# Optimization experiments

Measured on AMD Instinct MI355X. Metric: run time of the kernel, lower is better.

Reference implementation:

```python
import jax, jax.numpy as jnp
import numpy as np

B, P1, P2 = 16, 25, 24          # batch, patch-grid rows (+cls row), cols
E0, E1, E2 = 8, 8, 16           # 3-way factorized embed dim (total 1024)
H1, H2, H3 = 2, 2, 4            # 3-way head split (16 heads)
X, Y, Z = E0 // H1, E1 // H2, E2 // H3   # per-head factor dims (4,4,4)
SCALE = float((X * Y * Z) ** -0.5)        # head_dim = 64


def _tcl(x, w0, w1, w2, b):
    # Tensor Contraction Layer: mode-wise linear maps on the 3 embed modes.
    return jnp.einsum('bpqxyz,ax,cy,dz->bpqacd', x, w0, w1, w2) + b


def setup_inputs() -> dict:
    key = jax.random.key(0)
    ks = jax.random.split(key, 17)
    inp = {"x": jax.random.normal(ks[0], (B, P1, P2, E0, E1, E2), jnp.float32)}
    i = 1
    for nm in ("q", "k", "v", "o"):
        inp[f"{nm}_w0"] = jax.random.normal(ks[i], (E0, E0), jnp.float32) * (E0 ** -0.5); i += 1
        inp[f"{nm}_w1"] = jax.random.normal(ks[i], (E1, E1), jnp.float32) * (E1 ** -0.5); i += 1
        inp[f"{nm}_w2"] = jax.random.normal(ks[i], (E2, E2), jnp.float32) * (E2 ** -0.5); i += 1
        inp[f"{nm}_b"] = jax.random.normal(ks[i], (E0, E1, E2), jnp.float32) * 0.02; i += 1
    return inp


def _split_heads(t):
    t = t.reshape(B, P1, P2, X, H1, Y, H2, Z, H3)
    return t.transpose(0, 1, 2, 4, 6, 8, 3, 5, 7)


def reference(x,
              q_w0, q_w1, q_w2, q_b,
              k_w0, k_w1, k_w2, k_b,
              v_w0, v_w1, v_w2, v_b,
              o_w0, o_w1, o_w2, o_b):
    q = _tcl(x, q_w0, q_w1, q_w2, q_b)
    k = _tcl(x, k_w0, k_w1, k_w2, k_b)
    v = _tcl(x, v_w0, v_w1, v_w2, v_b)
    Q, K, V = _split_heads(q), _split_heads(k), _split_heads(v)
    # scores over all (p1,p2) x (m,n) token pairs, per (h1,h2,h3) head
    attn = jnp.einsum('bpqdefxyz,bmndefxyz->bdefpqmn', Q, K) * SCALE
    a = attn.reshape(B, H1, H2, H3, P1, P2, P1 * P2)
    a = jax.nn.softmax(a, axis=-1).reshape(attn.shape)
    out = jnp.einsum('bdefpqmn,bmndefxyz->bdefpqxyz', a, V)
    # b h1 h2 h3 p q x y z -> b p q (x h1)(y h2)(z h3)
    out = out.transpose(0, 4, 5, 6, 1, 7, 2, 8, 3).reshape(B, P1, P2, E0, E1, E2)
    return _tcl(out, o_w0, o_w1, o_w2, o_b)
```

## Files before the change

### kernel.cpp

```cpp
#include <hip/hip_runtime.h>

#define S   600
#define NB  16
#define NH  16
#define HD  64
#define QSCALE 0.18033688011112042f

#define LDT 20

typedef _Float16 f16x8 __attribute__((ext_vector_type(8)));
typedef float f32x4 __attribute__((ext_vector_type(4)));

__global__ __launch_bounds__(256) void tcl_qkv_kernel(
    const float* __restrict__ x,
    const float* __restrict__ qw0, const float* __restrict__ qw1,
    const float* __restrict__ qw2, const float* __restrict__ qb,
    const float* __restrict__ kw0, const float* __restrict__ kw1,
    const float* __restrict__ kw2, const float* __restrict__ kb,
    const float* __restrict__ vw0, const float* __restrict__ vw1,
    const float* __restrict__ vw2, const float* __restrict__ vb,
    _Float16* __restrict__ Qh, _Float16* __restrict__ Kh,
    _Float16* __restrict__ Vh)
{
  __shared__ __align__(16) float t1s[4][64 * LDT];
  __shared__ __align__(16) float t2s[4][64 * LDT];

  const int tid = threadIdx.x;
  const int wv = tid >> 6, lane = tid & 63;
  const int tok = blockIdx.x * 4 + wv;
  const int b = tok / S, t = tok - b * S;
  const int q = lane >> 3, zp = lane & 7;
  float* __restrict__ t1 = t1s[wv];
  float* __restrict__ t2 = t2s[wv];

  float2 xc[8];
  #pragma unroll
  for (int xx = 0; xx < 8; ++xx)
    xc[xx] = *(const float2*)&x[(size_t)tok * 1024 + xx * 128 + q * 16 + zp * 2];

  const int xs = lane >> 4;
  const int h1 = (lane >> 3) & 1;
  const int cc = lane & 7;
  const int ys = cc >> 1, h2 = cc & 1;

  const float* W0[3] = {qw0, kw0, vw0};
  const float* W1[3] = {qw1, kw1, vw1};
  const float* W2[3] = {qw2, kw2, vw2};
  const float* BB[3] = {qb, kb, vb};
  _Float16* OUT[3] = {Qh, Kh, Vh};

  #pragma unroll
  for (int p = 0; p < 3; ++p) {
    const float* __restrict__ w0 = W0[p];
    const float* __restrict__ w1 = W1[p];
    const float* __restrict__ w2 = W2[p];
    const float* __restrict__ bb = BB[p];
    _Float16* __restrict__ op = OUT[p];

    #pragma unroll
    for (int a = 0; a < 8; ++a) {
      float2 r = make_float2(0.f, 0.f);
      #pragma unroll
      for (int xx = 0; xx < 8; ++xx) {
        const float w = w0[a * 8 + xx];
        r.x = fmaf(w, xc[xx].x, r.x);
        r.y = fmaf(w, xc[xx].y, r.y);
      }
      *(float2*)&t1[(a * 8 + q) * LDT + zp * 2] = r;
    }
    __builtin_amdgcn_wave_barrier();

    float2 t1r[8];
    #pragma unroll
    for (int y = 0; y < 8; ++y)
      t1r[y] = *(float2*)&t1[(q * 8 + y) * LDT + zp * 2];
    #pragma unroll
    for (int c = 0; c < 8; ++c) {
      float2 r = make_float2(0.f, 0.f);
      #pragma unroll
      for (int y = 0; y < 8; ++y) {
        const float w = w1[c * 8 + y];
        r.x = fmaf(w, t1r[y].x, r.x);
        r.y = fmaf(w, t1r[y].y, r.y);
      }
      *(float2*)&t2[(q * 8 + c) * LDT + zp * 2] = r;
    }
    __builtin_amdgcn_wave_barrier();

    float t2r[16];
    #pragma unroll
    for (int k = 0; k < 4; ++k)
      *(float4*)&t2r[k * 4] = *(float4*)&t2[lane * LDT + k * 4];
    float bias[16];
    #pragma unroll
    for (int k = 0; k < 4; ++k)
      *(float4*)&bias[k * 4] = *(const float4*)&bb[lane * 16 + k * 4];
    float o[16];
    #pragma unroll
    for (int d = 0; d < 16; ++d) {
      float acc = 0.f;
      #pragma unroll
      for (int j = 0; j < 16; ++j)
        acc = fmaf(w2[d * 16 + j], t2r[j], acc);
      o[d] = acc + bias[d];
    }
    const float sc = (p == 0) ? QSCALE : 1.0f;
    #pragma unroll
    for (int h3 = 0; h3 < 4; ++h3) {
      union { _Float16 hh[4]; uint2 u; } pk;
      #pragma unroll
      for (int z = 0; z < 4; ++z)
        pk.hh[z] = (_Float16)(o[4 * z + h3] * sc);
      const int head = h1 * 8 + h2 * 4 + h3;
      *(uint2*)&op[((size_t)((b * NH + head) * S + t)) * HD + xs * 16 + ys * 4]
          = pk.u;
    }
    __builtin_amdgcn_wave_barrier();
  }
}

__global__ __launch_bounds__(256) void vtrans_kernel(
    const _Float16* __restrict__ Vh, _Float16* __restrict__ Vt)
{
  __shared__ __align__(16) _Float16 tile[64 * 64];
  const int tid = threadIdx.x;
  const int tt = blockIdx.x, h = blockIdx.y, b = blockIdx.z;
  const size_t rbase = (size_t)(b * NH + h) * S * HD;
  const size_t wbase = (size_t)(b * NH + h) * HD * S;
  const int t0 = tt * 64;

  #pragma unroll
  for (int hp = 0; hp < 2; ++hp) {
    const int u = hp * 256 + tid;
    const int r = u >> 3, ch = u & 7;
    f16x8 v = {0, 0, 0, 0, 0, 0, 0, 0};
    if (t0 + r < S) v = *(const f16x8*)&Vh[rbase + (size_t)(t0 + r) * HD + ch * 8];
    *(f16x8*)&tile[r * 64 + ((ch ^ ((r ^ (r >> 3)) & 7)) * 8)] = v;
  }
  __syncthreads();
  #pragma unroll
  for (int hp = 0; hp < 2; ++hp) {
    const int w = hp * 256 + tid;
    const int d = w >> 3, tc = w & 7;
    if (t0 + tc * 8 + 8 <= S) {
      const int cd = d >> 3;
      union { _Float16 hh[8]; f16x8 v; } g;
      #pragma unroll
      for (int e = 0; e < 8; ++e) {
        const int r = tc * 8 + e;
        g.hh[e] = tile[r * 64 + ((cd ^ ((r ^ (r >> 3)) & 7)) * 8) + (d & 7)];
      }
      *(f16x8*)&Vt[wbase + (size_t)d * S + t0 + tc * 8] = g.v;
    }
  }
}

template<bool TAIL>
__device__ __forceinline__ void attn_step(
    const _Float16* __restrict__ Ks, const _Float16* __restrict__ Vs,
    _Float16* __restrict__ Pw,
    const f16x8 qf0, const f16x8 qf1,
    f32x4 (&po)[4], float& mrow, float& lrow,
    const int lr, const int lg)
{
  constexpr int NMT = TAIL ? 2 : 4;
  f32x4 accs[NMT];
  #pragma unroll
  for (int mt = 0; mt < NMT; ++mt) accs[mt] = (f32x4){0.f, 0.f, 0.f, 0.f};
  #pragma unroll
  for (int c = 0; c < 2; ++c) {
    const f16x8 qf = c ? qf1 : qf0;
    #pragma unroll
    for (int mt = 0; mt < NMT; ++mt) {
      const int krow = mt * 16 + lr;
      const f16x8 kf = *(const f16x8*)
          &Ks[krow * 64 + (((4 * c + lg) ^ (krow & 7)) * 8)];
      accs[mt] = __builtin_amdgcn_mfma_f32_16x16x32_f16(kf, qf, accs[mt], 0, 0, 0);
    }
  }
  float sv[NMT][4];
  #pragma unroll
  for (int mt = 0; mt < NMT; ++mt)
    #pragma unroll
    for (int r = 0; r < 4; ++r) {
      float s = accs[mt][r];
      if (TAIL && mt == 1) s = (lg < 2) ? s : -1e30f;
      sv[mt][r] = s;
    }
  float tmax;
  {
    const float a = fmaxf(fmaxf(sv[0][0], sv[0][1]), fmaxf(sv[0][2], sv[0][3]));
    const float b = fmaxf(fmaxf(sv[1][0], sv[1][1]), fmaxf(sv[1][2], sv[1][3]));
    if (TAIL) {
      tmax = fmaxf(a, b);
    } else {
      const float c2 = fmaxf(fmaxf(sv[2][0], sv[2][1]), fmaxf(sv[2][2], sv[2][3]));
      const float d2 = fmaxf(fmaxf(sv[3][0], sv[3][1]), fmaxf(sv[3][2], sv[3][3]));
      tmax = fmaxf(fmaxf(a, b), fmaxf(c2, d2));
    }
  }
  tmax = fmaxf(tmax, __shfl_xor(tmax, 16));
  tmax = fmaxf(tmax, __shfl_xor(tmax, 32));
  if (!__all(tmax - mrow <= 11.0f)) {
    const float mn = fmaxf(mrow, tmax);
    const float corr = __builtin_amdgcn_exp2f(mrow - mn);
    lrow *= corr;
    #pragma unroll
    for (int dt = 0; dt < 4; ++dt) {
      po[dt][0] *= corr; po[dt][1] *= corr;
      po[dt][2] *= corr; po[dt][3] *= corr;
    }
    mrow = mn;
  }
  _Float16 ph[NMT][4];
  float rsv[NMT];
  #pragma unroll
  for (int mt = 0; mt < NMT; ++mt) {
    const float e0 = __builtin_amdgcn_exp2f(sv[mt][0] - mrow);
    const float e1 = __builtin_amdgcn_exp2f(sv[mt][1] - mrow);
    const float e2 = __builtin_amdgcn_exp2f(sv[mt][2] - mrow);
    const float e3 = __builtin_amdgcn_exp2f(sv[mt][3] - mrow);
    ph[mt][0] = (_Float16)e0; ph[mt][1] = (_Float16)e1;
    ph[mt][2] = (_Float16)e2; ph[mt][3] = (_Float16)e3;
    rsv[mt] = (e0 + e1) + (e2 + e3);
  }
  float rs = TAIL ? (rsv[0] + rsv[1]) : ((rsv[0] + rsv[1]) + (rsv[2] + rsv[3]));
  rs += __shfl_xor(rs, 16);
  rs += __shfl_xor(rs, 32);
  lrow += rs;
  #pragma unroll
  for (int mt = 0; mt < NMT; ++mt) {
    union { _Float16 hh[4]; unsigned long long u; } pk;
    pk.hh[0] = ph[mt][0]; pk.hh[1] = ph[mt][1];
    pk.hh[2] = ph[mt][2]; pk.hh[3] = ph[mt][3];
    const int idx = lr * 64 + (((2 * mt + (lg >> 1)) ^ (lr & 7)) * 8)
                  + (lg & 1) * 4;
    *(unsigned long long*)&Pw[idx] = pk.u;
  }
  __builtin_amdgcn_wave_barrier();
  #pragma unroll
  for (int c = 0; c < (TAIL ? 1 : 2); ++c) {
    const f16x8 pf = *(const f16x8*)&Pw[lr * 64 + (((4 * c + lg) ^ (lr & 7)) * 8)];
    #pragma unroll
    for (int dt = 0; dt < 4; ++dt) {
      const int drow = dt * 16 + lr;
      const f16x8 vf = *(const f16x8*)
          &Vs[drow * 64 + (((4 * c + lg) ^ (drow & 7)) * 8)];
      po[dt] = __builtin_amdgcn_mfma_f32_16x16x32_f16(vf, pf, po[dt], 0, 0, 0);
    }
  }
}

__global__ __launch_bounds__(256) void attn_mfma_kernel(
    const _Float16* __restrict__ Qh, const _Float16* __restrict__ Kh,
    const _Float16* __restrict__ Vt, float* __restrict__ Og)
{
  __shared__ __align__(16) union {
    struct {
      _Float16 K[2][64 * 64];
      _Float16 V[2][64 * 64];
      _Float16 P[4][16 * 64];
    } m;
    float ot[4][64 * 17];
  } sm;

  const int tid = threadIdx.x;
  const int lane = tid & 63;
  const int wv = tid >> 6;
  const int id = blockIdx.x;
  const int idx = id >> 3;
  const int bh = (id & 7) * 32 + idx / 10;
  const int qt = idx - (idx / 10) * 10;
  const size_t base  = (size_t)bh * S * HD;
  const size_t vbase = (size_t)bh * HD * S;
  const int lr = lane & 15;
  const int lg = lane >> 4;

  const int qrow_l = qt * 64 + wv * 16 + lr;
  const int qrow = (qrow_l < S) ? qrow_l : (S - 1);
  const f16x8 qf0 = *(const f16x8*)&Qh[base + (size_t)qrow * HD + lg * 8];
  const f16x8 qf1 = *(const f16x8*)&Qh[base + (size_t)qrow * HD + 32 + lg * 8];

  f32x4 po[4] = {{0.f,0.f,0.f,0.f},{0.f,0.f,0.f,0.f},
                 {0.f,0.f,0.f,0.f},{0.f,0.f,0.f,0.f}};
  float mrow = -1e30f, lrow = 0.f;

  const int srow = tid >> 3, sch = tid & 7;
  const int sswz = ((sch ^ (srow & 7)) * 8);
  const int srow2 = (256 + tid) >> 3;
  const int sswz2 = ((sch ^ (srow2 & 7)) * 8);

  auto stage_load = [&](int kt, f16x8* kv, f16x8* vv) {
    const int kb = kt * 64;
    f16x8 z = {0, 0, 0, 0, 0, 0, 0, 0};
    kv[0] = z; kv[1] = z; vv[0] = z; vv[1] = z;
    if (kb + srow  < S) kv[0] = *(const f16x8*)&Kh[base + (size_t)(kb + srow ) * HD + sch * 8];
    if (kb + srow2 < S) kv[1] = *(const f16x8*)&Kh[base + (size_t)(kb + srow2) * HD + sch * 8];
    if (kb + sch * 8 + 8 <= S) {
      vv[0] = *(const f16x8*)&Vt[vbase + (size_t)srow  * S + kb + sch * 8];
      vv[1] = *(const f16x8*)&Vt[vbase + (size_t)srow2 * S + kb + sch * 8];
    }
  };
  auto stage_write = [&](int buf, const f16x8* kv, const f16x8* vv) {
    *(f16x8*)&sm.m.K[buf][srow  * 64 + sswz ] = kv[0];
    *(f16x8*)&sm.m.K[buf][srow2 * 64 + sswz2] = kv[1];
    *(f16x8*)&sm.m.V[buf][srow  * 64 + sswz ] = vv[0];
    *(f16x8*)&sm.m.V[buf][srow2 * 64 + sswz2] = vv[1];
  };

  f16x8 kv[2], vv[2];
  stage_load(0, kv, vv);
  stage_write(0, kv, vv);
  __syncthreads();

  #pragma unroll 1
  for (int kt = 0; kt < 9; ++kt) {
    const int cur = kt & 1;
    stage_load(kt + 1, kv, vv);
    attn_step<false>(&sm.m.K[cur][0], &sm.m.V[cur][0], &sm.m.P[wv][0],
                     qf0, qf1, po, mrow, lrow, lr, lg);
    stage_write(cur ^ 1, kv, vv);
    __syncthreads();
  }
  attn_step<true>(&sm.m.K[1][0], &sm.m.V[1][0], &sm.m.P[wv][0],
                  qf0, qf1, po, mrow, lrow, lr, lg);
  __syncthreads();

  const float invl = 1.0f / lrow;
  #pragma unroll
  for (int dt = 0; dt < 4; ++dt)
    #pragma unroll
    for (int r = 0; r < 4; ++r)
      sm.ot[wv][(dt * 16 + 4 * lg + r) * 17 + lr] = po[dt][r] * invl;
  __builtin_amdgcn_wave_barrier();
  #pragma unroll
  for (int ps = 0; ps < 4; ++ps) {
    const int qr = ps * 4 + lg;
    const int gq = qt * 64 + wv * 16 + qr;
    if (gq < S) {
      const int d0 = lr * 4;
      float4 o4;
      o4.x = sm.ot[wv][(d0 + 0) * 17 + qr];
      o4.y = sm.ot[wv][(d0 + 1) * 17 + qr];
      o4.z = sm.ot[wv][(d0 + 2) * 17 + qr];
      o4.w = sm.ot[wv][(d0 + 3) * 17 + qr];
      *(float4*)&Og[base + (size_t)gq * HD + d0] = o4;
    }
  }
}

__global__ __launch_bounds__(256) void tcl_out_kernel(
    const float* __restrict__ Og,
    const float* __restrict__ ow0, const float* __restrict__ ow1,
    const float* __restrict__ ow2, const float* __restrict__ ob,
    float* __restrict__ out)
{
  __shared__ __align__(16) float t1s[4][64 * LDT];
  __shared__ __align__(16) float t2s[4][64 * LDT];

  const int tid = threadIdx.x;
  const int wv = tid >> 6, lane = tid & 63;
  const int tok = blockIdx.x * 4 + wv;
  const int b = tok / S, t = tok - b * S;
  const int q = lane >> 3, zp = lane & 7;
  float* __restrict__ t1 = t1s[wv];
  float* __restrict__ t2 = t2s[wv];

  float2 xc[8];
  {
    const int h2g = q & 1, yg = q >> 1;
    const int h3g = 2 * (zp & 1), zg = zp >> 1;
    #pragma unroll
    for (int xx = 0; xx < 8; ++xx) {
      const int headb = (xx & 1) * 8 + h2g * 4 + h3g;
      const size_t off = ((size_t)((b * NH + headb) * S + t)) * HD
                       + (xx >> 1) * 16 + yg * 4 + zg;
      xc[xx].x = Og[off];
      xc[xx].y = Og[off + (size_t)S * HD];
    }
  }

  #pragma unroll
  for (int a = 0; a < 8; ++a) {
    float2 r = make_float2(0.f, 0.f);
    #pragma unroll
    for (int xx = 0; xx < 8; ++xx) {
      const float w = ow0[a * 8 + xx];
      r.x = fmaf(w, xc[xx].x, r.x);
      r.y = fmaf(w, xc[xx].y, r.y);
    }
    *(float2*)&t1[(a * 8 + q) * LDT + zp * 2] = r;
  }
  __builtin_amdgcn_wave_barrier();

  float2 t1r[8];
  #pragma unroll
  for (int y = 0; y < 8; ++y)
    t1r[y] = *(float2*)&t1[(q * 8 + y) * LDT + zp * 2];
  #pragma unroll
  for (int c = 0; c < 8; ++c) {
    float2 r = make_float2(0.f, 0.f);
    #pragma unroll
    for (int y = 0; y < 8; ++y) {
      const float w = ow1[c * 8 + y];
      r.x = fmaf(w, t1r[y].x, r.x);
      r.y = fmaf(w, t1r[y].y, r.y);
    }
    *(float2*)&t2[(q * 8 + c) * LDT + zp * 2] = r;
  }
  __builtin_amdgcn_wave_barrier();

  float t2r[16];
  #pragma unroll
  for (int k = 0; k < 4; ++k)
    *(float4*)&t2r[k * 4] = *(float4*)&t2[lane * LDT + k * 4];
  float bias[16];
  #pragma unroll
  for (int k = 0; k < 4; ++k)
    *(float4*)&bias[k * 4] = *(const float4*)&ob[lane * 16 + k * 4];
  float o[16];
  #pragma unroll
  for (int d = 0; d < 16; ++d) {
    float acc = 0.f;
    #pragma unroll
    for (int j = 0; j < 16; ++j)
      acc = fmaf(ow2[d * 16 + j], t2r[j], acc);
    o[d] = acc + bias[d];
  }
  #pragma unroll
  for (int k = 0; k < 4; ++k) {
    const float4 res = make_float4(o[4 * k], o[4 * k + 1],
                                   o[4 * k + 2], o[4 * k + 3]);
    *(float4*)&out[(size_t)tok * 1024 + lane * 16 + k * 4] = res;
  }
}

extern "C" void kernel_launch(void* const* d_in, const int* in_sizes, int n_in,
                              void* d_out, int out_size, void* d_ws, size_t ws_size,
                              hipStream_t stream) {
  const float* x   = (const float*)d_in[0];
  const float* qw0 = (const float*)d_in[1];
  const float* qw1 = (const float*)d_in[2];
  const float* qw2 = (const float*)d_in[3];
  const float* qb  = (const float*)d_in[4];
  const float* kw0 = (const float*)d_in[5];
  const float* kw1 = (const float*)d_in[6];
  const float* kw2 = (const float*)d_in[7];
  const float* kb  = (const float*)d_in[8];
  const float* vw0 = (const float*)d_in[9];
  const float* vw1 = (const float*)d_in[10];
  const float* vw2 = (const float*)d_in[11];
  const float* vb  = (const float*)d_in[12];
  const float* ow0 = (const float*)d_in[13];
  const float* ow1 = (const float*)d_in[14];
  const float* ow2 = (const float*)d_in[15];
  const float* ob  = (const float*)d_in[16];

  const size_t N = (size_t)NB * NH * S * HD;
  _Float16* Qh  = (_Float16*)d_ws;
  _Float16* Kh  = Qh + N;
  _Float16* Vth = Kh + N;
  _Float16* Vh  = Vth + N;
  float*    O   = (float*)Vh;

  tcl_qkv_kernel<<<dim3(NB * S / 4), 256, 0, stream>>>(
      x, qw0, qw1, qw2, qb, kw0, kw1, kw2, kb, vw0, vw1, vw2, vb, Qh, Kh, Vh);
  vtrans_kernel<<<dim3(10, NH, NB), 256, 0, stream>>>(Vh, Vth);
  attn_mfma_kernel<<<dim3(2560), 256, 0, stream>>>(Qh, Kh, Vth, O);
  tcl_out_kernel<<<dim3(NB * S / 4), 256, 0, stream>>>(O, ow0, ow1, ow2, ob,
                                                       (float*)d_out);
}
```

Baseline: 126.7 us.

## Single-buffer K/V LDS staging with register prefetch and MFMA priority hints

Replaces the double-buffered K/V shared-memory tiles with a single buffer. Each iteration now writes the register-prefetched tile, issues the next global load, and synchronises twice before computing. Full tiles are loaded without per-element bounds checks, with a separate tail loader for the last partial tile. Raises wave priority around the MFMA blocks via s_setprio. This halves K/V LDS use, which may raise occupancy, at the cost of an extra barrier per iteration and less overlap between LDS writes and compute.

```diff
diff --git a/kernel.cpp b/kernel.cpp
--- a/kernel.cpp
+++ b/kernel.cpp
@@ -167,6 +167,7 @@
   f32x4 accs[NMT];
   #pragma unroll
   for (int mt = 0; mt < NMT; ++mt) accs[mt] = (f32x4){0.f, 0.f, 0.f, 0.f};
+  __builtin_amdgcn_s_setprio(1);
   #pragma unroll
   for (int c = 0; c < 2; ++c) {
     const f16x8 qf = c ? qf1 : qf0;
@@ -178,6 +179,7 @@
       accs[mt] = __builtin_amdgcn_mfma_f32_16x16x32_f16(kf, qf, accs[mt], 0, 0, 0);
     }
   }
+  __builtin_amdgcn_s_setprio(0);
   float sv[NMT][4];
   #pragma unroll
   for (int mt = 0; mt < NMT; ++mt)
@@ -238,6 +240,7 @@
     *(unsigned long long*)&Pw[idx] = pk.u;
   }
   __builtin_amdgcn_wave_barrier();
+  __builtin_amdgcn_s_setprio(1);
   #pragma unroll
   for (int c = 0; c < (TAIL ? 1 : 2); ++c) {
     const f16x8 pf = *(const f16x8*)&Pw[lr * 64 + (((4 * c + lg) ^ (lr & 7)) * 8)];
@@ -249,6 +252,7 @@
       po[dt] = __builtin_amdgcn_mfma_f32_16x16x32_f16(vf, pf, po[dt], 0, 0, 0);
     }
   }
+  __builtin_amdgcn_s_setprio(0);
 }
 
 __global__ __launch_bounds__(256) void attn_mfma_kernel(
@@ -257,8 +261,8 @@
 {
   __shared__ __align__(16) union {
     struct {
-      _Float16 K[2][64 * 64];
-      _Float16 V[2][64 * 64];
+      _Float16 K[64 * 64];
+      _Float16 V[64 * 64];
       _Float16 P[4][16 * 64];
     } m;
     float ot[4][64 * 17];
@@ -286,43 +290,50 @@
   float mrow = -1e30f, lrow = 0.f;
 
   const int srow = tid >> 3, sch = tid & 7;
+  const int srow2 = srow + 32;
   const int sswz = ((sch ^ (srow & 7)) * 8);
-  const int srow2 = (256 + tid) >> 3;
-  const int sswz2 = ((sch ^ (srow2 & 7)) * 8);
-
-  auto stage_load = [&](int kt, f16x8* kv, f16x8* vv) {
+
+  f16x8 kv[2], vv[2];
+  auto stage_load_full = [&](int kt) {
     const int kb = kt * 64;
-    f16x8 z = {0, 0, 0, 0, 0, 0, 0, 0};
-    kv[0] = z; kv[1] = z; vv[0] = z; vv[1] = z;
-    if (kb + srow  < S) kv[0] = *(const f16x8*)&Kh[base + (size_t)(kb + srow ) * HD + sch * 8];
-    if (kb + srow2 < S) kv[1] = *(const f16x8*)&Kh[base + (size_t)(kb + srow2) * HD + sch * 8];
-    if (kb + sch * 8 + 8 <= S) {
+    kv[0] = *(const f16x8*)&Kh[base + (size_t)(kb + srow ) * HD + sch * 8];
+    kv[1] = *(const f16x8*)&Kh[base + (size_t)(kb + srow2) * HD + sch * 8];
+    vv[0] = *(const f16x8*)&Vt[vbase + (size_t)srow  * S + kb + sch * 8];
+    vv[1] = *(const f16x8*)&Vt[vbase + (size_t)srow2 * S + kb + sch * 8];
+  };
+  auto stage_load_tail = [&]() {
+    const int kb = 576;
+    const f16x8 z = {0, 0, 0, 0, 0, 0, 0, 0};
+    kv[0] = (srow < 24)
+        ? *(const f16x8*)&Kh[base + (size_t)(kb + srow) * HD + sch * 8] : z;
+    kv[1] = z;
+    if (sch < 3) {
       vv[0] = *(const f16x8*)&Vt[vbase + (size_t)srow  * S + kb + sch * 8];
       vv[1] = *(const f16x8*)&Vt[vbase + (size_t)srow2 * S + kb + sch * 8];
-    }
+    } else { vv[0] = z; vv[1] = z; }
   };
-  auto stage_write = [&](int buf, const f16x8* kv, const f16x8* vv) {
-    *(f16x8*)&sm.m.K[buf][srow  * 64 + sswz ] = kv[0];
-    *(f16x8*)&sm.m.K[buf][srow2 * 64 + sswz2] = kv[1];
-    *(f16x8*)&sm.m.V[buf][srow  * 64 + sswz ] = vv[0];
-    *(f16x8*)&sm.m.V[buf][srow2 * 64 + sswz2] = vv[1];
+  auto stage_write = [&]() {
+    *(f16x8*)&sm.m.K[srow  * 64 + sswz] = kv[0];
+    *(f16x8*)&sm.m.K[srow2 * 64 + sswz] = kv[1];
+    *(f16x8*)&sm.m.V[srow  * 64 + sswz] = vv[0];
+    *(f16x8*)&sm.m.V[srow2 * 64 + sswz] = vv[1];
   };
 
-  f16x8 kv[2], vv[2];
-  stage_load(0, kv, vv);
-  stage_write(0, kv, vv);
-  __syncthreads();
-
+  stage_load_full(0);
   #pragma unroll 1
   for (int kt = 0; kt < 9; ++kt) {
-    const int cur = kt & 1;
-    stage_load(kt + 1, kv, vv);
-    attn_step<false>(&sm.m.K[cur][0], &sm.m.V[cur][0], &sm.m.P[wv][0],
+    __syncthreads();
+    stage_write();
+    if (kt < 8) stage_load_full(kt + 1);
+    else        stage_load_tail();
+    __syncthreads();
+    attn_step<false>(&sm.m.K[0], &sm.m.V[0], &sm.m.P[wv][0],
                      qf0, qf1, po, mrow, lrow, lr, lg);
-    stage_write(cur ^ 1, kv, vv);
-    __syncthreads();
-  }
-  attn_step<true>(&sm.m.K[1][0], &sm.m.V[1][0], &sm.m.P[wv][0],
+  }
+  __syncthreads();
+  stage_write();
+  __syncthreads();
+  attn_step<true>(&sm.m.K[0], &sm.m.V[0], &sm.m.P[wv][0],
                   qf0, qf1, po, mrow, lrow, lr, lg);
   __syncthreads();
 
```

Result: no change. 125.4 us (-1.0%).

## Stream K/V tiles straight into LDS with global_load_lds and raise MFMA priority

Applied to the files above, without the earlier changes.

The attention kernel now loads K and V tiles with the global-to-LDS DMA intrinsic instead of staging them through registers. The swizzle moves to the global source address so the LDS layout stays the same. It also brackets the MFMA sections with s_setprio, adds a min-blocks launch bound and unrolls the tile loop by two. The aim is to cut register pressure and VALU/LDS store work in the staging path and overlap the copies with compute. In exchange, the last tile reads past the sequence end without bounds checks: the V tail is zeroed explicitly, and K relies on score masking.

```diff
diff --git a/kernel.cpp b/kernel.cpp
--- a/kernel.cpp
+++ b/kernel.cpp
@@ -155,6 +155,12 @@
   }
 }
 
+__device__ __forceinline__ void gload16(const _Float16* g, _Float16* l) {
+  __builtin_amdgcn_global_load_lds(
+      (const __attribute__((address_space(1))) unsigned int*)g,
+      (__attribute__((address_space(3))) unsigned int*)l, 16, 0, 0);
+}
+
 template<bool TAIL>
 __device__ __forceinline__ void attn_step(
     const _Float16* __restrict__ Ks, const _Float16* __restrict__ Vs,
@@ -167,6 +173,7 @@
   f32x4 accs[NMT];
   #pragma unroll
   for (int mt = 0; mt < NMT; ++mt) accs[mt] = (f32x4){0.f, 0.f, 0.f, 0.f};
+  __builtin_amdgcn_s_setprio(1);
   #pragma unroll
   for (int c = 0; c < 2; ++c) {
     const f16x8 qf = c ? qf1 : qf0;
@@ -178,6 +185,7 @@
       accs[mt] = __builtin_amdgcn_mfma_f32_16x16x32_f16(kf, qf, accs[mt], 0, 0, 0);
     }
   }
+  __builtin_amdgcn_s_setprio(0);
   float sv[NMT][4];
   #pragma unroll
   for (int mt = 0; mt < NMT; ++mt)
@@ -238,6 +246,7 @@
     *(unsigned long long*)&Pw[idx] = pk.u;
   }
   __builtin_amdgcn_wave_barrier();
+  __builtin_amdgcn_s_setprio(1);
   #pragma unroll
   for (int c = 0; c < (TAIL ? 1 : 2); ++c) {
     const f16x8 pf = *(const f16x8*)&Pw[lr * 64 + (((4 * c + lg) ^ (lr & 7)) * 8)];
@@ -249,9 +258,10 @@
       po[dt] = __builtin_amdgcn_mfma_f32_16x16x32_f16(vf, pf, po[dt], 0, 0, 0);
     }
   }
-}
-
-__global__ __launch_bounds__(256) void attn_mfma_kernel(
+  __builtin_amdgcn_s_setprio(0);
+}
+
+__global__ __launch_bounds__(256, 4) void attn_mfma_kernel(
     const _Float16* __restrict__ Qh, const _Float16* __restrict__ Kh,
     const _Float16* __restrict__ Vt, float* __restrict__ Og)
 {
@@ -285,43 +295,38 @@
                  {0.f,0.f,0.f,0.f},{0.f,0.f,0.f,0.f}};
   float mrow = -1e30f, lrow = 0.f;
 
-  const int srow = tid >> 3, sch = tid & 7;
-  const int sswz = ((sch ^ (srow & 7)) * 8);
-  const int srow2 = (256 + tid) >> 3;
-  const int sswz2 = ((sch ^ (srow2 & 7)) * 8);
-
-  auto stage_load = [&](int kt, f16x8* kv, f16x8* vv) {
+  const int sr = lane >> 3, ss = lane & 7;
+  const int swz8 = (ss ^ sr) * 8;
+  const int c0 = wv, c1 = wv + 4;
+  const _Float16* kg0 = Kh + base + (size_t)(c0 * 8 + sr) * HD + swz8;
+  const _Float16* kg1 = Kh + base + (size_t)(c1 * 8 + sr) * HD + swz8;
+  const _Float16* vg0 = Vt + vbase + (size_t)(c0 * 8 + sr) * S + swz8;
+  const _Float16* vg1 = Vt + vbase + (size_t)(c1 * 8 + sr) * S + swz8;
+
+  auto gload_tile = [&](int kt, int b) {
     const int kb = kt * 64;
-    f16x8 z = {0, 0, 0, 0, 0, 0, 0, 0};
-    kv[0] = z; kv[1] = z; vv[0] = z; vv[1] = z;
-    if (kb + srow  < S) kv[0] = *(const f16x8*)&Kh[base + (size_t)(kb + srow ) * HD + sch * 8];
-    if (kb + srow2 < S) kv[1] = *(const f16x8*)&Kh[base + (size_t)(kb + srow2) * HD + sch * 8];
-    if (kb + sch * 8 + 8 <= S) {
-      vv[0] = *(const f16x8*)&Vt[vbase + (size_t)srow  * S + kb + sch * 8];
-      vv[1] = *(const f16x8*)&Vt[vbase + (size_t)srow2 * S + kb + sch * 8];
-    }
+    gload16(kg0 + (size_t)kb * HD, &sm.m.K[b][c0 * 512]);
+    gload16(kg1 + (size_t)kb * HD, &sm.m.K[b][c1 * 512]);
+    gload16(vg0 + kb, &sm.m.V[b][c0 * 512]);
+    gload16(vg1 + kb, &sm.m.V[b][c1 * 512]);
   };
-  auto stage_write = [&](int buf, const f16x8* kv, const f16x8* vv) {
-    *(f16x8*)&sm.m.K[buf][srow  * 64 + sswz ] = kv[0];
-    *(f16x8*)&sm.m.K[buf][srow2 * 64 + sswz2] = kv[1];
-    *(f16x8*)&sm.m.V[buf][srow  * 64 + sswz ] = vv[0];
-    *(f16x8*)&sm.m.V[buf][srow2 * 64 + sswz2] = vv[1];
-  };
-
-  f16x8 kv[2], vv[2];
-  stage_load(0, kv, vv);
-  stage_write(0, kv, vv);
+
+  gload_tile(0, 0);
+  #pragma unroll 2
+  for (int kt = 0; kt < 9; ++kt) {
+    const int b = kt & 1;
+    __syncthreads();
+    gload_tile(kt + 1, b ^ 1);
+    attn_step<false>(&sm.m.K[b][0], &sm.m.V[b][0], &sm.m.P[wv][0],
+                     qf0, qf1, po, mrow, lrow, lr, lg);
+  }
   __syncthreads();
-
-  #pragma unroll 1
-  for (int kt = 0; kt < 9; ++kt) {
-    const int cur = kt & 1;
-    stage_load(kt + 1, kv, vv);
-    attn_step<false>(&sm.m.K[cur][0], &sm.m.V[cur][0], &sm.m.P[wv][0],
-                     qf0, qf1, po, mrow, lrow, lr, lg);
-    stage_write(cur ^ 1, kv, vv);
-    __syncthreads();
-  }
+  for (int u = tid; u < 320; u += 256) {
+    const int row = u / 5, kc = 3 + u % 5;
+    *(f16x8*)&sm.m.V[1][row * 64 + ((kc ^ (row & 7)) * 8)] =
+        (f16x8){0, 0, 0, 0, 0, 0, 0, 0};
+  }
+  __syncthreads();
   attn_step<true>(&sm.m.K[1][0], &sm.m.V[1][0], &sm.m.P[wv][0],
                   qf0, qf1, po, mrow, lrow, lr, lg);
   __syncthreads();
```

After: 119.1 us. 6.0% less time.
